# Kernel tuning notes

Hardware: AMD Instinct MI355X
Metric: run time of the kernel (lower is better)

The kernel has to match this reference:

```python
import jax, jax.numpy as jnp
import numpy as np
from jax import lax

N, C_IN, C_OUT, H, W, K = 32, 512, 512, 56, 56, 7


def setup_inputs() -> dict:
    key = jax.random.key(0)
    ks = jax.random.split(key, 7)
    s_in = 1.0 / np.sqrt(C_IN)
    s_out = 1.0 / np.sqrt(C_OUT)
    return {
        "x": jax.random.normal(ks[0], (N, C_IN, H, W), dtype=jnp.float32),
        "k": K,
        "w_up": jax.random.normal(ks[1], (C_OUT, C_IN), dtype=jnp.float32) * s_in,
        "b_up": jax.random.normal(ks[2], (C_OUT,), dtype=jnp.float32) * s_in,
        "w_down": jax.random.normal(ks[3], (C_OUT, C_IN), dtype=jnp.float32) * s_in,
        "b_down": jax.random.normal(ks[4], (C_OUT,), dtype=jnp.float32) * s_in,
        "w_final": jax.random.normal(ks[5], (C_OUT, C_OUT), dtype=jnp.float32) * s_out,
        "b_final": jax.random.normal(ks[6], (C_OUT,), dtype=jnp.float32) * s_out,
    }


def _conv1x1(x, w, b):
    # x: [N, Cin, H, W], w: [Cout, Cin] -> [N, Cout, H, W]
    return jnp.einsum("nchw,oc->nohw", x, w) + b[None, :, None, None]


def reference(x, k, w_up, b_up, w_down, b_down, w_final, b_final):
    n, c_in, h, w = x.shape
    c_out = w_up.shape[0]
    pad = (k - 1) // 2

    up = _conv1x1(x, w_up, b_up)  # [N, Cout, H, W]

    # AdaptiveAvgPool2d(k): H, W divisible by k -> exact uniform pooling
    pooled = x.reshape(n, c_in, k, h // k, k, w // k).mean(axis=(3, 5))  # [N, Cin, k, k]
    down = _conv1x1(pooled, w_down, b_down)  # [N, Cout, k, k] dynamic depthwise kernels

    def dw_conv(u, ker):
        # u: [Cout, H, W], ker: [Cout, k, k]; depthwise (groups = Cout)
        return lax.conv_general_dilated(
            u[None],                    # [1, Cout, H, W]
            ker[:, None],               # [Cout, 1, k, k] (OIHW)
            window_strides=(1, 1),
            padding=[(pad, pad), (pad, pad)],
            feature_group_count=c_out,
            dimension_numbers=("NCHW", "OIHW", "NCHW"),
        )[0]

    out = jax.vmap(dw_conv)(up, down)  # [N, Cout, H, W]
    return _conv1x1(out, w_final, b_final)
```

## Files before the change

kernel.cpp:

```cpp
#include <hip/hip_runtime.h>
#include <hip/hip_bf16.h>

typedef unsigned short u16;
typedef _Float16 f16x8 __attribute__((ext_vector_type(8)));
typedef _Float16 half2v __attribute__((ext_vector_type(2)));
typedef float f32x4 __attribute__((ext_vector_type(4)));
typedef unsigned short ushortx8 __attribute__((ext_vector_type(8)));

#define GPTR(p)  ((const __attribute__((address_space(1))) void*)(p))
#define LDSPTR(p) ((__attribute__((address_space(3))) void*)(p))

static __device__ __forceinline__ u16 f2h(float f) {
    _Float16 h = (_Float16)f;
    union { _Float16 h; u16 u; } v; v.h = h; return v.u;
}

__global__ __launch_bounds__(256) void cvtw_kernel(
    const float* __restrict__ wu, const float* __restrict__ wf,
    u16* __restrict__ wub, u16* __restrict__ wfb) {
    int i = blockIdx.x * 256 + threadIdx.x;
    wub[i] = f2h(wu[i]);
    wfb[i] = f2h(wf[i]);
}

__global__ __launch_bounds__(256) void transpose_kernel(
    const float* __restrict__ x, u16* __restrict__ xt) {
    __shared__ float tile[64][65];
    int bid = blockIdx.x;
    int jt = bid % 49;
    int r = bid / 49;
    int ct = r & 7, n = r >> 3;
    const float* src = x + ((size_t)(n * 512 + ct * 64)) * 3136 + jt * 64;
    for (int e = threadIdx.x; e < 4096; e += 256) {
        int i = e >> 6, jj = e & 63;
        tile[i][jj] = src[(size_t)i * 3136 + jj];
    }
    __syncthreads();
    u16* dst = xt + ((size_t)(n * 3136 + jt * 64)) * 512 + ct * 64;
    for (int e = threadIdx.x; e < 2048; e += 256) {
        int jj = e >> 5, i2 = (e & 31) * 2;
        unsigned int val = (unsigned)f2h(tile[i2][jj]) | ((unsigned)f2h(tile[i2 + 1][jj]) << 16);
        *(unsigned int*)(dst + (size_t)jj * 512 + i2) = val;
    }
}

__global__ __launch_bounds__(256) void poolh_kernel(
    const u16* __restrict__ xt, float* __restrict__ pooled) {
    int bid = blockIdx.x;
    int n = bid / 49, cell = bid - n * 49;
    int py = cell / 7, px = cell - py * 7;
    int t = threadIdx.x;
    float s0 = 0.f, s1 = 0.f;
    for (int r = 0; r < 8; ++r) {
        int h = py * 8 + r;
        const u16* base = xt + ((size_t)(n * 3136 + h * 56 + px * 8)) * 512 + 2 * t;
        #pragma unroll
        for (int cc = 0; cc < 8; ++cc) {
            half2v v = *(const half2v*)(base + (size_t)cc * 512);
            s0 += (float)v[0]; s1 += (float)v[1];
        }
    }
    float* pp = pooled + (size_t)n * 512 * 49 + py * 7 + px;
    pp[(size_t)(2 * t) * 49]     = s0 * (1.f / 64.f);
    pp[(size_t)(2 * t + 1) * 49] = s1 * (1.f / 64.f);
}

__global__ __launch_bounds__(256) void down_kernel(
    const float* __restrict__ pooled, const float* __restrict__ w_down,
    const float* __restrict__ b_down, float* __restrict__ down) {
    int bid = blockIdx.x;
    int n = bid >> 5, og = bid & 31;
    int wv = threadIdx.x >> 6, lane = threadIdx.x & 63;
    int o0 = og * 16 + wv * 4;
    const float* pp = pooled + (size_t)n * 512 * 49;
    const float* w0 = w_down + (size_t)o0 * 512;
    float a0 = 0, a1 = 0, a2 = 0, a3 = 0;
    int cell = lane < 49 ? lane : 48;
    #pragma unroll 4
    for (int c = 0; c < 512; ++c) {
        float p = pp[c * 49 + cell];
        a0 += p * w0[c];
        a1 += p * w0[512 + c];
        a2 += p * w0[1024 + c];
        a3 += p * w0[1536 + c];
    }
    if (lane < 49) {
        float* dd = down + ((size_t)n * 512 + o0) * 49 + lane;
        dd[0]   = a0 + b_down[o0];
        dd[49]  = a1 + b_down[o0 + 1];
        dd[98]  = a2 + b_down[o0 + 2];
        dd[147] = a3 + b_down[o0 + 3];
    }
}

template <int EPI>
__global__ __launch_bounds__(256) void gemm_kernel(
    const u16* __restrict__ A, const u16* __restrict__ Bt,
    const float* __restrict__ bias, void* __restrict__ Cout) {
    constexpr int K = 512;
    __shared__ u16 As[128 * 32];
    __shared__ u16 Bs[128 * 32];
    int tid = threadIdx.x, wv = tid >> 6, lane = tid & 63;
    int bid = blockIdx.x;
    int tm, tn;
    if (EPI == 0) { tm = bid >> 2; tn = bid & 3; }
    else          { tm = bid & 3;  tn = bid >> 2; }
    size_t m0 = (size_t)tm * 128, n0 = (size_t)tn * 128;
    int lr = lane & 15, lk = (lane >> 4) * 8;
    int wr = wv >> 1, wc = wv & 1;

    int e0 = wv * 512 + lane * 8;
    int e1 = e0 + 2048;
    const u16* pa0 = A + (m0 + (size_t)(e0 >> 5)) * K + (e0 & 31);
    const u16* pa1 = A + (m0 + (size_t)(e1 >> 5)) * K + (e1 & 31);
    const u16* pb0 = Bt + (n0 + (size_t)(e0 >> 5)) * K + (e0 & 31);
    const u16* pb1 = Bt + (n0 + (size_t)(e1 >> 5)) * K + (e1 & 31);
    u16* sa0 = &As[wv * 512]; u16* sa1 = &As[wv * 512 + 2048];
    u16* sb0 = &Bs[wv * 512]; u16* sb1 = &Bs[wv * 512 + 2048];

    f32x4 acc[4][4] = {};

    for (int kt = 0; kt < K / 32; ++kt) {
        __builtin_amdgcn_global_load_lds(GPTR(pa0), LDSPTR(sa0), 16, 0, 0);
        __builtin_amdgcn_global_load_lds(GPTR(pa1), LDSPTR(sa1), 16, 0, 0);
        __builtin_amdgcn_global_load_lds(GPTR(pb0), LDSPTR(sb0), 16, 0, 0);
        __builtin_amdgcn_global_load_lds(GPTR(pb1), LDSPTR(sb1), 16, 0, 0);
        pa0 += 32; pa1 += 32; pb0 += 32; pb1 += 32;
        __syncthreads();
        f16x8 af[4], bfr[4];
        #pragma unroll
        for (int mi = 0; mi < 4; ++mi)
            af[mi] = *(const f16x8*)&As[(wr * 64 + mi * 16 + lr) * 32 + lk];
        #pragma unroll
        for (int ni = 0; ni < 4; ++ni)
            bfr[ni] = *(const f16x8*)&Bs[(wc * 64 + ni * 16 + lr) * 32 + lk];
        #pragma unroll
        for (int mi = 0; mi < 4; ++mi)
            #pragma unroll
            for (int ni = 0; ni < 4; ++ni)
                acc[mi][ni] = __builtin_amdgcn_mfma_f32_16x16x32_f16(af[mi], bfr[ni], acc[mi][ni], 0, 0, 0);
        __syncthreads();
    }

    if (EPI == 0) {
        u16* C = (u16*)Cout;
        #pragma unroll
        for (int ni = 0; ni < 4; ++ni) {
            size_t col = n0 + wc * 64 + ni * 16 + lr;
            float bv = bias[col];
            #pragma unroll
            for (int mi = 0; mi < 4; ++mi) {
                size_t row = m0 + wr * 64 + mi * 16 + (lane >> 4) * 4;
                #pragma unroll
                for (int r = 0; r < 4; ++r)
                    C[(row + r) * 512 + col] = f2h(acc[mi][ni][r] + bv);
            }
        }
    } else {
        float* C = (float*)Cout;
        #pragma unroll
        for (int ni = 0; ni < 4; ++ni) {
            int col = (int)(n0 + wc * 64 + ni * 16 + lr);
            int nimg = col / 3136;
            int jj = col - nimg * 3136;
            size_t obase = (size_t)nimg * 512 * 3136 + jj;
            #pragma unroll
            for (int mi = 0; mi < 4; ++mi) {
                int row = (int)(m0 + wr * 64 + mi * 16 + (lane >> 4) * 4);
                #pragma unroll
                for (int r = 0; r < 4; ++r)
                    C[obase + (size_t)(row + r) * 3136] = acc[mi][ni][r] + bias[row + r];
            }
        }
    }
}

__global__ __launch_bounds__(256) void dw_kernel(
    const u16* __restrict__ up, const float* __restrict__ down,
    u16* __restrict__ dw) {
    __shared__ u16 tile[16 * 898];
    int bid = blockIdx.x;
    int n = bid / 224;
    int rem = bid - n * 224;
    int rt = rem >> 5;
    int cg = rem & 31;
    int tid = threadIdx.x;

    for (int e = tid; e < 1736; e += 256) {
        int p = e >> 1, q = e & 1;
        int hh = p / 62, wcol = p - hh * 62;
        int h = rt * 8 + hh - 3, w = wcol - 3;
        ushortx8 v = (ushortx8)0;
        if (h >= 0 && h < 56 && (unsigned)w < 56u)
            v = *(const ushortx8*)(up + ((size_t)(n * 3136 + h * 56 + w)) * 512 + cg * 16 + q * 8);
        #pragma unroll
        for (int j = 0; j < 8; ++j)
            tile[(q * 8 + j) * 898 + hh * 64 + wcol] = (u16)v[j];
    }

    int c = tid & 15, u = tid >> 4;
    int row = u >> 1, sh = u & 1;
    const float* kp = down + ((size_t)n * 512 + cg * 16 + c) * 49;
    half2v ke[7][4], ko[7][4];
    #pragma unroll
    for (int ky = 0; ky < 7; ++ky) {
        float k0 = kp[ky*7+0], k1 = kp[ky*7+1], k2 = kp[ky*7+2], k3 = kp[ky*7+3];
        float k4 = kp[ky*7+4], k5 = kp[ky*7+5], k6 = kp[ky*7+6];
        ke[ky][0] = half2v{(_Float16)k0, (_Float16)k1};
        ke[ky][1] = half2v{(_Float16)k2, (_Float16)k3};
        ke[ky][2] = half2v{(_Float16)k4, (_Float16)k5};
        ke[ky][3] = half2v{(_Float16)k6, (_Float16)0.f};
        ko[ky][0] = half2v{(_Float16)0.f, (_Float16)k0};
        ko[ky][1] = half2v{(_Float16)k1, (_Float16)k2};
        ko[ky][2] = half2v{(_Float16)k3, (_Float16)k4};
        ko[ky][3] = half2v{(_Float16)k5, (_Float16)k6};
    }
    __syncthreads();

    const u16* plane = &tile[c * 898];
    for (int s2 = 0; s2 < 2; ++s2) {
        int seg = sh * 2 + s2;
        int o0 = seg * 14;
        float acc[14] = {0,0,0,0,0,0,0,0,0,0,0,0,0,0};
        #pragma unroll
        for (int ky = 0; ky < 7; ++ky) {
            const u16* rp = plane + (row + ky) * 64 + o0;
            half2v w2[10];
            #pragma unroll
            for (int t = 0; t < 10; ++t) w2[t] = *(const half2v*)(rp + t * 2);
            #pragma unroll
            for (int m = 0; m < 7; ++m) {
                float ae = acc[2*m], ao = acc[2*m+1];
                ae = __builtin_amdgcn_fdot2(w2[m],   ke[ky][0], ae, false);
                ae = __builtin_amdgcn_fdot2(w2[m+1], ke[ky][1], ae, false);
                ae = __builtin_amdgcn_fdot2(w2[m+2], ke[ky][2], ae, false);
                ae = __builtin_amdgcn_fdot2(w2[m+3], ke[ky][3], ae, false);
                ao = __builtin_amdgcn_fdot2(w2[m],   ko[ky][0], ao, false);
                ao = __builtin_amdgcn_fdot2(w2[m+1], ko[ky][1], ao, false);
                ao = __builtin_amdgcn_fdot2(w2[m+2], ko[ky][2], ao, false);
                ao = __builtin_amdgcn_fdot2(w2[m+3], ko[ky][3], ao, false);
                acc[2*m] = ae; acc[2*m+1] = ao;
            }
        }
        int h = rt * 8 + row;
        u16* op = dw + ((size_t)(n * 3136 + h * 56 + o0)) * 512 + cg * 16 + c;
        #pragma unroll
        for (int i = 0; i < 14; ++i)
            op[(size_t)i * 512] = f2h(acc[i]);
    }
}

extern "C" void kernel_launch(void* const* d_in, const int* in_sizes, int n_in,
                              void* d_out, int out_size, void* d_ws, size_t ws_size,
                              hipStream_t stream) {
    const float* x       = (const float*)d_in[0];
    const float* w_up    = (const float*)d_in[2];
    const float* b_up    = (const float*)d_in[3];
    const float* w_down  = (const float*)d_in[4];
    const float* b_down  = (const float*)d_in[5];
    const float* w_final = (const float*)d_in[6];
    const float* b_final = (const float*)d_in[7];

    char* ws = (char*)d_ws;
    u16*   xt     = (u16*)  (ws + 0);
    u16*   up     = (u16*)  (ws + 102760448);
    float* pooled = (float*)(ws + 205520896);
    float* down   = (float*)(ws + 208732160);
    u16*   wub    = (u16*)  (ws + 211943424);
    u16*   wfb    = (u16*)  (ws + 212467712);
    u16*   dwb    = xt;

    cvtw_kernel<<<1024, 256, 0, stream>>>(w_up, w_final, wub, wfb);
    transpose_kernel<<<12544, 256, 0, stream>>>(x, xt);
    poolh_kernel<<<1568, 256, 0, stream>>>(xt, pooled);
    down_kernel<<<1024, 256, 0, stream>>>(pooled, w_down, b_down, down);
    gemm_kernel<0><<<3136, 256, 0, stream>>>(xt, wub, b_up, up);
    dw_kernel<<<7168, 256, 0, stream>>>(up, down, dwb);
    gemm_kernel<1><<<3136, 256, 0, stream>>>(wfb, dwb, b_final, d_out);
}
```

Baseline: 487.7 us.

## Blocked 8-pixel layout for up tensor, vectorized dw tile loads, swizzled GEMM tile order

The up-projection GEMM now writes its fp16 output in a blocked layout of 8 consecutive pixels per channel, stored as packed 4-element vectors. The depthwise kernel then loads each channel row as contiguous 16-byte vectors straight into LDS instead of scattering single halves. The depthwise kernel also computes 28 outputs per thread in one pass with wraparound indexing into a zero-padded row, and both GEMMs use a grouped block-to-tile mapping intended to improve L2 reuse. The costs are more register pressure from 28 accumulators and subtle index math around the padding and wraparound.

```diff
diff --git a/kernel.cpp b/kernel.cpp
--- a/kernel.cpp
+++ b/kernel.cpp
@@ -3,9 +3,11 @@
 
 typedef unsigned short u16;
 typedef _Float16 f16x8 __attribute__((ext_vector_type(8)));
+typedef _Float16 f16x4 __attribute__((ext_vector_type(4)));
 typedef _Float16 half2v __attribute__((ext_vector_type(2)));
 typedef float f32x4 __attribute__((ext_vector_type(4)));
 typedef unsigned short ushortx8 __attribute__((ext_vector_type(8)));
+typedef unsigned short ushortx4 __attribute__((ext_vector_type(4)));
 
 #define GPTR(p)  ((const __attribute__((address_space(1))) void*)(p))
 #define LDSPTR(p) ((__attribute__((address_space(3))) void*)(p))
@@ -103,8 +105,8 @@
     int tid = threadIdx.x, wv = tid >> 6, lane = tid & 63;
     int bid = blockIdx.x;
     int tm, tn;
-    if (EPI == 0) { tm = bid >> 2; tn = bid & 3; }
-    else          { tm = bid & 3;  tn = bid >> 2; }
+    if (EPI == 0) { tm = (bid >> 5) * 8 + (bid & 7); tn = (bid >> 3) & 3; }
+    else          { tn = (bid >> 5) * 8 + (bid & 7); tm = (bid >> 3) & 3; }
     size_t m0 = (size_t)tm * 128, n0 = (size_t)tn * 128;
     int lr = lane & 15, lk = (lane >> 4) * 8;
     int wr = wv >> 1, wc = wv & 1;
@@ -150,10 +152,12 @@
             float bv = bias[col];
             #pragma unroll
             for (int mi = 0; mi < 4; ++mi) {
-                size_t row = m0 + wr * 64 + mi * 16 + (lane >> 4) * 4;
+                size_t rowb = m0 + wr * 64 + mi * 16 + (lane >> 4) * 4;
+                ushortx4 pack;
                 #pragma unroll
                 for (int r = 0; r < 4; ++r)
-                    C[(row + r) * 512 + col] = f2h(acc[mi][ni][r] + bv);
+                    pack[r] = f2h(acc[mi][ni][r] + bv);
+                *(ushortx4*)&C[(rowb >> 3) * 4096 + col * 8 + (rowb & 7)] = pack;
             }
         }
     } else {
@@ -176,9 +180,9 @@
 }
 
 __global__ __launch_bounds__(256) void dw_kernel(
-    const u16* __restrict__ up, const float* __restrict__ down,
+    const u16* __restrict__ upb, const float* __restrict__ down,
     u16* __restrict__ dw) {
-    __shared__ u16 tile[16 * 898];
+    __shared__ u16 tile[14 * 16 * 72];
     int bid = blockIdx.x;
     int n = bid / 224;
     int rem = bid - n * 224;
@@ -186,68 +190,74 @@
     int cg = rem & 31;
     int tid = threadIdx.x;
 
-    for (int e = tid; e < 1736; e += 256) {
-        int p = e >> 1, q = e & 1;
-        int hh = p / 62, wcol = p - hh * 62;
-        int h = rt * 8 + hh - 3, w = wcol - 3;
+    if (tid < 224)
+        *(ushortx8*)&tile[tid * 72 + 56] = (ushortx8)0;
+
+    for (int e = tid; e < 1568; e += 256) {
+        int c = e & 15;
+        int p = e >> 4;
+        int hh = p / 7, jb = p - hh * 7;
+        int h = rt * 8 + hh - 3;
         ushortx8 v = (ushortx8)0;
-        if (h >= 0 && h < 56 && (unsigned)w < 56u)
-            v = *(const ushortx8*)(up + ((size_t)(n * 3136 + h * 56 + w)) * 512 + cg * 16 + q * 8);
-        #pragma unroll
-        for (int j = 0; j < 8; ++j)
-            tile[(q * 8 + j) * 898 + hh * 64 + wcol] = (u16)v[j];
+        if ((unsigned)h < 56u)
+            v = *(const ushortx8*)(upb + ((size_t)(n * 392 + h * 7 + jb)) * 4096 + (cg * 16 + c) * 8);
+        *(ushortx8*)&tile[(hh * 16 + c) * 72 + jb * 8] = v;
     }
 
     int c = tid & 15, u = tid >> 4;
-    int row = u >> 1, sh = u & 1;
+    int row = u >> 1, wh = u & 1, w0 = wh * 28;
     const float* kp = down + ((size_t)n * 512 + cg * 16 + c) * 49;
-    half2v ke[7][4], ko[7][4];
+    half2v kE[7][4], kO[7][4];
     #pragma unroll
     for (int ky = 0; ky < 7; ++ky) {
         float k0 = kp[ky*7+0], k1 = kp[ky*7+1], k2 = kp[ky*7+2], k3 = kp[ky*7+3];
         float k4 = kp[ky*7+4], k5 = kp[ky*7+5], k6 = kp[ky*7+6];
-        ke[ky][0] = half2v{(_Float16)k0, (_Float16)k1};
-        ke[ky][1] = half2v{(_Float16)k2, (_Float16)k3};
-        ke[ky][2] = half2v{(_Float16)k4, (_Float16)k5};
-        ke[ky][3] = half2v{(_Float16)k6, (_Float16)0.f};
-        ko[ky][0] = half2v{(_Float16)0.f, (_Float16)k0};
-        ko[ky][1] = half2v{(_Float16)k1, (_Float16)k2};
-        ko[ky][2] = half2v{(_Float16)k3, (_Float16)k4};
-        ko[ky][3] = half2v{(_Float16)k5, (_Float16)k6};
+        kE[ky][0] = half2v{(_Float16)0.f, (_Float16)k0};
+        kE[ky][1] = half2v{(_Float16)k1,  (_Float16)k2};
+        kE[ky][2] = half2v{(_Float16)k3,  (_Float16)k4};
+        kE[ky][3] = half2v{(_Float16)k5,  (_Float16)k6};
+        kO[ky][0] = half2v{(_Float16)k0,  (_Float16)k1};
+        kO[ky][1] = half2v{(_Float16)k2,  (_Float16)k3};
+        kO[ky][2] = half2v{(_Float16)k4,  (_Float16)k5};
+        kO[ky][3] = half2v{(_Float16)k6,  (_Float16)0.f};
     }
     __syncthreads();
 
-    const u16* plane = &tile[c * 898];
-    for (int s2 = 0; s2 < 2; ++s2) {
-        int seg = sh * 2 + s2;
-        int o0 = seg * 14;
-        float acc[14] = {0,0,0,0,0,0,0,0,0,0,0,0,0,0};
-        #pragma unroll
-        for (int ky = 0; ky < 7; ++ky) {
-            const u16* rp = plane + (row + ky) * 64 + o0;
-            half2v w2[10];
-            #pragma unroll
-            for (int t = 0; t < 10; ++t) w2[t] = *(const half2v*)(rp + t * 2);
-            #pragma unroll
-            for (int m = 0; m < 7; ++m) {
-                float ae = acc[2*m], ao = acc[2*m+1];
-                ae = __builtin_amdgcn_fdot2(w2[m],   ke[ky][0], ae, false);
-                ae = __builtin_amdgcn_fdot2(w2[m+1], ke[ky][1], ae, false);
-                ae = __builtin_amdgcn_fdot2(w2[m+2], ke[ky][2], ae, false);
-                ae = __builtin_amdgcn_fdot2(w2[m+3], ke[ky][3], ae, false);
-                ao = __builtin_amdgcn_fdot2(w2[m],   ko[ky][0], ao, false);
-                ao = __builtin_amdgcn_fdot2(w2[m+1], ko[ky][1], ao, false);
-                ao = __builtin_amdgcn_fdot2(w2[m+2], ko[ky][2], ao, false);
-                ao = __builtin_amdgcn_fdot2(w2[m+3], ko[ky][3], ao, false);
-                acc[2*m] = ae; acc[2*m+1] = ao;
-            }
-        }
-        int h = rt * 8 + row;
-        u16* op = dw + ((size_t)(n * 3136 + h * 56 + o0)) * 512 + cg * 16 + c;
-        #pragma unroll
-        for (int i = 0; i < 14; ++i)
-            op[(size_t)i * 512] = f2h(acc[i]);
-    }
+    float acc[28];
+    #pragma unroll
+    for (int i = 0; i < 28; ++i) acc[i] = 0.f;
+
+    #pragma unroll
+    for (int ky = 0; ky < 7; ++ky) {
+        const u16* rp = &tile[((row + ky) * 16 + c) * 72];
+        half2v w2[18];
+        #pragma unroll
+        for (int t = 0; t < 9; ++t) {
+            int p0 = ((w0 >> 1) - 2 + 2 * t) & 31;
+            f16x4 q = *(const f16x4*)(rp + p0 * 2);
+            w2[2*t]   = half2v{q[0], q[1]};
+            w2[2*t+1] = half2v{q[2], q[3]};
+        }
+        #pragma unroll
+        for (int m = 0; m < 14; ++m) {
+            float ae = acc[2*m], ao = acc[2*m+1];
+            ae = __builtin_amdgcn_fdot2(w2[m],   kE[ky][0], ae, false);
+            ae = __builtin_amdgcn_fdot2(w2[m+1], kE[ky][1], ae, false);
+            ae = __builtin_amdgcn_fdot2(w2[m+2], kE[ky][2], ae, false);
+            ae = __builtin_amdgcn_fdot2(w2[m+3], kE[ky][3], ae, false);
+            ao = __builtin_amdgcn_fdot2(w2[m+1], kO[ky][0], ao, false);
+            ao = __builtin_amdgcn_fdot2(w2[m+2], kO[ky][1], ao, false);
+            ao = __builtin_amdgcn_fdot2(w2[m+3], kO[ky][2], ao, false);
+            ao = __builtin_amdgcn_fdot2(w2[m+4], kO[ky][3], ao, false);
+            acc[2*m] = ae; acc[2*m+1] = ao;
+        }
+    }
+
+    int h = rt * 8 + row;
+    u16* op = dw + ((size_t)(n * 3136 + h * 56 + w0)) * 512 + cg * 16 + c;
+    #pragma unroll
+    for (int i = 0; i < 28; ++i)
+        op[(size_t)i * 512] = f2h(acc[i]);
 }
 
 extern "C" void kernel_launch(void* const* d_in, const int* in_sizes, int n_in,
@@ -263,7 +273,7 @@
 
     char* ws = (char*)d_ws;
     u16*   xt     = (u16*)  (ws + 0);
-    u16*   up     = (u16*)  (ws + 102760448);
+    u16*   upb    = (u16*)  (ws + 102760448);
     float* pooled = (float*)(ws + 205520896);
     float* down   = (float*)(ws + 208732160);
     u16*   wub    = (u16*)  (ws + 211943424);
@@ -274,7 +284,7 @@
     transpose_kernel<<<12544, 256, 0, stream>>>(x, xt);
     poolh_kernel<<<1568, 256, 0, stream>>>(xt, pooled);
     down_kernel<<<1024, 256, 0, stream>>>(pooled, w_down, b_down, down);
-    gemm_kernel<0><<<3136, 256, 0, stream>>>(xt, wub, b_up, up);
-    dw_kernel<<<7168, 256, 0, stream>>>(up, down, dwb);
+    gemm_kernel<0><<<3136, 256, 0, stream>>>(xt, wub, b_up, upb);
+    dw_kernel<<<7168, 256, 0, stream>>>(upb, down, dwb);
     gemm_kernel<1><<<3136, 256, 0, stream>>>(wfb, dwb, b_final, d_out);
 }
```

Result: faster. 410.6 us (-15.8%).
